# Optimization experiments

Hardware: AMD Instinct MI355X
Metric: run time of the kernel (lower is better)

Reference implementation:

```python
import math
import jax, jax.numpy as jnp
import numpy as np

L, H, C, T = 6, 16, 1024, 256   # layers, heads, n_embd, context steps (seq = 3T)
NACT, D_FF, B = 80, 4096, 4

def _conv(x, w, b, s, p):
    y = jax.lax.conv_general_dilated(x, w, (s, s), [(p, p), (p, p)],
                                     dimension_numbers=('NCHW', 'OIHW', 'NCHW'))
    return y + b[None, :, None, None]

def _ln(x, g, b):
    m = x.mean(-1, keepdims=True)
    v = ((x - m) ** 2).mean(-1, keepdims=True)
    return (x - m) / jnp.sqrt(v + 1e-5) * g + b

def _forward(states, rtgs, meta_states, circuit_feas,
             conv1_w, conv1_b, conv2_w, conv2_b, conv3_w, conv3_b,
             enc_w, enc_b, meta_w1, meta_b1, meta_w2, meta_b2,
             ret_w, ret_b, act_emb, pos_emb, gpos_emb,
             ln1_g, ln1_b, ln2_g, ln2_b,
             Wq, bq, Wk, bk, Wv, bv, Wo, bo,
             Wm1, bm1, Wm2, bm2, lnf_g, lnf_b, head_w,
             actions, timesteps):
    Bb, Tl = states.shape[0], states.shape[1]
    # state CNN encoder: (B*T, 8, 8, 10) -> 16 feats -> Linear(16, C-4)
    s = states.reshape(-1, 8, 8, 10)
    h = jax.nn.relu(_conv(s, conv1_w, conv1_b, 2, 1))
    h = jax.nn.relu(_conv(h, conv2_w, conv2_b, 2, 1))
    h = jax.nn.relu(_conv(h, conv3_w, conv3_b, 2, 1))
    se = h.reshape(h.shape[0], -1) @ enc_w + enc_b                    # (B*T, C-4)
    me = jax.nn.relu(meta_states.reshape(-1, 4) @ meta_w1 + meta_b1) @ meta_w2 + meta_b2
    state_emb = jnp.tanh(jnp.concatenate([se, me], axis=1)).reshape(Bb, Tl, C)
    # circuit embedding is computed then zeroed in source (no_circuit_emb=True) -> no effect
    rtg_emb = jnp.tanh(rtgs @ ret_w + ret_b)                          # (B, T, C)
    act_e = act_emb[actions[..., 0]]                                  # (B, T, C)
    # interleave (rtg, state, action) per timestep -> (B, 3T, C)
    tok = jnp.stack([rtg_emb, state_emb, act_e], axis=2).reshape(Bb, 3 * Tl, C)
    pos = gpos_emb[0, timesteps[:, 0, 0]][:, None, :] + pos_emb[:, :3 * Tl, :]
    x = tok + pos
    mask = jnp.tril(jnp.ones((3 * Tl, 3 * Tl), bool))
    d = C // H
    for i in range(L):
        hx = _ln(x, ln1_g[i], ln1_b[i])
        q = (hx @ Wq[i] + bq[i]).reshape(Bb, 3 * Tl, H, d)
        k = (hx @ Wk[i] + bk[i]).reshape(Bb, 3 * Tl, H, d)
        v = (hx @ Wv[i] + bv[i]).reshape(Bb, 3 * Tl, H, d)
        att = jnp.einsum('bqhd,bkhd->bhqk', q, k) / math.sqrt(d)
        att = jax.nn.softmax(jnp.where(mask, att, -jnp.inf), axis=-1)
        y = jnp.einsum('bhqk,bkhd->bqhd', att, v).reshape(Bb, 3 * Tl, C)
        x = x + (y @ Wo[i] + bo[i])
        h2 = _ln(x, ln2_g[i], ln2_b[i])
        x = x + (jax.nn.gelu(h2 @ Wm1[i] + bm1[i], approximate=False) @ Wm2[i] + bm2[i])
    logits = _ln(x, lnf_g, lnf_b) @ head_w                            # (B, 3T, NACT)
    return logits[:, 1::3, :]                                         # predictions at state tokens

def setup_inputs():
    ks = iter(jax.random.split(jax.random.key(0), 64))
    def W(*shape):
        return jax.random.normal(next(ks), shape, jnp.float32) * 0.02
    return {
        'states': jax.random.normal(next(ks), (B, T, 640), jnp.float32),
        'rtgs': jax.random.normal(next(ks), (B, T, 1), jnp.float32),
        'meta_states': jax.random.normal(next(ks), (B, T, 4), jnp.float32),
        'circuit_feas': jax.random.normal(next(ks), (B, 768), jnp.float32),
        'conv1_w': W(16, 8, 8, 8), 'conv1_b': jnp.zeros(16),
        'conv2_w': W(32, 16, 4, 4), 'conv2_b': jnp.zeros(32),
        'conv3_w': W(16, 32, 3, 3), 'conv3_b': jnp.zeros(16),
        'enc_w': W(16, C - 4), 'enc_b': jnp.zeros(C - 4),
        'meta_w1': W(4, 32), 'meta_b1': jnp.zeros(32),
        'meta_w2': W(32, 4), 'meta_b2': jnp.zeros(4),
        'ret_w': W(1, C), 'ret_b': jnp.zeros(C),
        'act_emb': W(NACT, C),
        'pos_emb': W(1, 3 * T + 1, C), 'gpos_emb': W(1, T + 1, C),
        'ln1_g': jnp.ones((L, C)), 'ln1_b': jnp.zeros((L, C)),
        'ln2_g': jnp.ones((L, C)), 'ln2_b': jnp.zeros((L, C)),
        'Wq': W(L, C, C), 'bq': jnp.zeros((L, C)),
        'Wk': W(L, C, C), 'bk': jnp.zeros((L, C)),
        'Wv': W(L, C, C), 'bv': jnp.zeros((L, C)),
        'Wo': W(L, C, C), 'bo': jnp.zeros((L, C)),
        'Wm1': W(L, C, D_FF), 'bm1': jnp.zeros((L, D_FF)),
        'Wm2': W(L, D_FF, C), 'bm2': jnp.zeros((L, C)),
        'lnf_g': jnp.ones(C), 'lnf_b': jnp.zeros(C),
        'head_w': W(C, NACT),
        'actions': jax.random.randint(next(ks), (B, T, 1), 0, NACT),
        'timesteps': jax.random.randint(next(ks), (B, 1, 1), 0, T + 1),
    }

def reference(states, rtgs, meta_states, circuit_feas,
              conv1_w, conv1_b, conv2_w, conv2_b, conv3_w, conv3_b,
              enc_w, enc_b, meta_w1, meta_b1, meta_w2, meta_b2,
              ret_w, ret_b, act_emb, pos_emb, gpos_emb,
              ln1_g, ln1_b, ln2_g, ln2_b,
              Wq, bq, Wk, bk, Wv, bv, Wo, bo,
              Wm1, bm1, Wm2, bm2, lnf_g, lnf_b, head_w,
              actions, timesteps):
    return _forward(states, rtgs, meta_states, circuit_feas,
                    conv1_w, conv1_b, conv2_w, conv2_b, conv3_w, conv3_b,
                    enc_w, enc_b, meta_w1, meta_b1, meta_w2, meta_b2,
                    ret_w, ret_b, act_emb, pos_emb, gpos_emb,
                    ln1_g, ln1_b, ln2_g, ln2_b,
                    Wq, bq, Wk, bk, Wv, bv, Wo, bo,
                    Wm1, bm1, Wm2, bm2, lnf_g, lnf_b, head_w,
                    actions, timesteps)
```

## Files before the change

### kernel.cpp

```cpp
#include <hip/hip_runtime.h>
#include <hip/hip_bf16.h>


#define S_LEN 768
#define C_DIM 1024
#define NHEAD 16
#define HDIM 64
#define BATCH 4
#define TCTX 256
#define DFF 4096
#define NACT 80
#define MROWS (BATCH * S_LEN)

typedef __attribute__((ext_vector_type(4))) float f32x4;
typedef __attribute__((ext_vector_type(8))) short bf16x8;
typedef __attribute__((ext_vector_type(8))) _Float16 f16x8;

static __device__ __forceinline__ unsigned short f2bf(float f) {
    unsigned int u = __float_as_uint(f);
    u += 0x7FFF + ((u >> 16) & 1);
    return (unsigned short)(u >> 16);
}
static __device__ __forceinline__ float bf2f(unsigned short h) {
    return __uint_as_float(((unsigned int)h) << 16);
}
static __device__ __forceinline__ unsigned short f2h(float f) {
    _Float16 h = (_Float16)f;
    return __builtin_bit_cast(unsigned short, h);
}

static __device__ __forceinline__ void gload16(void* l, const void* g) {
    __builtin_amdgcn_global_load_lds(
        (__attribute__((address_space(1))) void*)(g),
        (__attribute__((address_space(3))) void*)(l), 16, 0, 0);
}

__global__ __launch_bounds__(256) void transpose_w_kernel(
    const float* __restrict__ Wq, const float* __restrict__ Wk,
    const float* __restrict__ Wv, const float* __restrict__ Wo,
    const float* __restrict__ Wm1, const float* __restrict__ Wm2,
    unsigned short* __restrict__ Wb)
{
    const int t = blockIdx.x;
    const float* src; unsigned short* dst; int K, N, kt, nt;
    if (t < 1024) {
        const int m = t >> 8, tile = t & 255;
        src = (m == 0) ? Wq : (m == 1) ? Wk : (m == 2) ? Wv : Wo;
        dst = Wb + (size_t)m * 1048576;
        K = 1024; N = 1024; kt = tile >> 4; nt = tile & 15;
    } else if (t < 2048) {
        const int tile = t - 1024;
        src = Wm1; dst = Wb + (size_t)4 * 1048576;
        K = 1024; N = 4096; kt = tile >> 6; nt = tile & 63;
    } else {
        const int tile = t - 2048;
        src = Wm2; dst = Wb + (size_t)8 * 1048576;
        K = 4096; N = 1024; kt = tile >> 4; nt = tile & 15;
    }
    const int k0 = kt * 64, n0 = nt * 64;
    __shared__ float Ls[64][65];

    const int r = threadIdx.x >> 2, p = threadIdx.x & 3;
    #pragma unroll
    for (int i = 0; i < 4; ++i)
        *(float4*)&Ls[r][p * 16 + i * 4] =
            *(const float4*)&src[(size_t)(k0 + r) * N + n0 + p * 16 + i * 4];
    __syncthreads();

    unsigned short __align__(16) h[16];
    #pragma unroll
    for (int i = 0; i < 16; ++i) h[i] = f2bf(Ls[p * 16 + i][r]);
    unsigned short* d = dst + (size_t)(n0 + r) * K + k0 + p * 16;
    *(uint4*)d       = *(uint4*)&h[0];
    *(uint4*)(d + 8) = *(uint4*)&h[8];
}

__global__ __launch_bounds__(256) void embed_kernel(
    const float* __restrict__ states, const float* __restrict__ rtgs,
    const float* __restrict__ meta,
    const float* __restrict__ c1w, const float* __restrict__ c1b,
    const float* __restrict__ c2w, const float* __restrict__ c2b,
    const float* __restrict__ c3w, const float* __restrict__ c3b,
    const float* __restrict__ encw, const float* __restrict__ encb,
    const float* __restrict__ mw1, const float* __restrict__ mb1,
    const float* __restrict__ mw2, const float* __restrict__ mb2,
    const float* __restrict__ retw, const float* __restrict__ retb,
    const float* __restrict__ aemb, const float* __restrict__ pos,
    const float* __restrict__ gpos,
    const int* __restrict__ actions, const int* __restrict__ timesteps,
    float* __restrict__ X)
{
    const int n = blockIdx.x;
    const int b = n >> 8, t = n & 255;
    const int tid = threadIdx.x;

    __shared__ float sin_[640];
    __shared__ float h1[96];
    __shared__ float h2[32];
    __shared__ float feat[16];
    __shared__ float hidm[32];
    __shared__ float mer[4];

    for (int e = tid; e < 640; e += 256)
        sin_[e] = states[(size_t)n * 640 + e];
    __syncthreads();

    if (tid < 96) {
        int o = tid / 6, rem = tid % 6, oh = rem / 3, ow = rem % 3;
        float a = c1b[o];
        for (int ci = 0; ci < 8; ++ci)
            for (int kh = 0; kh < 8; ++kh) {
                int ih = oh * 2 - 1 + kh;
                if (ih < 0 || ih >= 8) continue;
                for (int kw = 0; kw < 8; ++kw) {
                    int iw = ow * 2 - 1 + kw;
                    if (iw < 0 || iw >= 10) continue;
                    a += c1w[((o * 8 + ci) * 8 + kh) * 8 + kw] * sin_[ci * 80 + ih * 10 + iw];
                }
            }
        h1[tid] = fmaxf(a, 0.f);
    }
    if (tid < 32) {
        float a = mb1[tid];
        for (int i = 0; i < 4; ++i)
            a += meta[(size_t)n * 4 + i] * mw1[i * 32 + tid];
        hidm[tid] = fmaxf(a, 0.f);
    }
    __syncthreads();

    if (tid < 32) {
        float a = c2b[tid];
        for (int ci = 0; ci < 16; ++ci)
            for (int kh = 0; kh < 4; ++kh) {
                int ih = -1 + kh;
                if (ih < 0 || ih >= 2) continue;
                for (int kw = 0; kw < 4; ++kw) {
                    int iw = -1 + kw;
                    if (iw < 0 || iw >= 3) continue;
                    a += c2w[((tid * 16 + ci) * 4 + kh) * 4 + kw] * h1[ci * 6 + ih * 3 + iw];
                }
            }
        h2[tid] = fmaxf(a, 0.f);
    }
    __syncthreads();

    if (tid < 16) {
        float a = c3b[tid];
        for (int ci = 0; ci < 32; ++ci)
            a += c3w[(tid * 32 + ci) * 9 + 4] * h2[ci];
        feat[tid] = fmaxf(a, 0.f);
    }
    if (tid < 4) {
        float a = mb2[tid];
        for (int j = 0; j < 32; ++j) a += hidm[j] * mw2[j * 4 + tid];
        mer[tid] = a;
    }
    __syncthreads();

    const float r = rtgs[n];
    const int a_idx = actions[n];
    const int g = timesteps[b];
    const size_t xbase = ((size_t)b * S_LEN + 3 * t) * C_DIM;

    for (int c = tid; c < C_DIM; c += 256) {
        float se;
        if (c < 1020) {
            float acc = encb[c];
            #pragma unroll
            for (int k = 0; k < 16; ++k) acc += feat[k] * encw[k * 1020 + c];
            se = acc;
        } else {
            se = mer[c - 1020];
        }
        const float st = tanhf(se);
        const float rt = tanhf(r * retw[c] + retb[c]);
        const float ae = aemb[(size_t)a_idx * C_DIM + c];
        const float gp = gpos[(size_t)g * C_DIM + c];
        X[xbase + c]             = rt + gp + pos[(size_t)(3 * t + 0) * C_DIM + c];
        X[xbase + C_DIM + c]     = st + gp + pos[(size_t)(3 * t + 1) * C_DIM + c];
        X[xbase + 2 * C_DIM + c] = ae + gp + pos[(size_t)(3 * t + 2) * C_DIM + c];
    }
}

__global__ __launch_bounds__(256) void ln_bf16_kernel(
    const float* __restrict__ in, unsigned short* __restrict__ out,
    const float* __restrict__ gw, const float* __restrict__ bw)
{
    const int row = blockIdx.x * 4 + (threadIdx.x >> 6);
    const int lane = threadIdx.x & 63;
    const float* x = in + (size_t)row * C_DIM;

    float4 v[4];
    float s = 0.f;
    #pragma unroll
    for (int j = 0; j < 4; ++j) {
        v[j] = *(const float4*)&x[lane * 4 + j * 256];
        s += (v[j].x + v[j].y) + (v[j].z + v[j].w);
    }
    #pragma unroll
    for (int o = 1; o < 64; o <<= 1) s += __shfl_xor(s, o, 64);
    const float mean = s * (1.0f / 1024.0f);

    float s2 = 0.f;
    #pragma unroll
    for (int j = 0; j < 4; ++j) {
        float dx = v[j].x - mean, dy = v[j].y - mean;
        float dz = v[j].z - mean, dw = v[j].w - mean;
        s2 += (dx * dx + dy * dy) + (dz * dz + dw * dw);
    }
    #pragma unroll
    for (int o = 1; o < 64; o <<= 1) s2 += __shfl_xor(s2, o, 64);
    const float inv = rsqrtf(s2 * (1.0f / 1024.0f) + 1e-5f);

    #pragma unroll
    for (int j = 0; j < 4; ++j) {
        const int c = lane * 4 + j * 256;
        ushort4 o4;
        o4.x = f2bf((v[j].x - mean) * inv * gw[c + 0] + bw[c + 0]);
        o4.y = f2bf((v[j].y - mean) * inv * gw[c + 1] + bw[c + 1]);
        o4.z = f2bf((v[j].z - mean) * inv * gw[c + 2] + bw[c + 2]);
        o4.w = f2bf((v[j].w - mean) * inv * gw[c + 3] + bw[c + 3]);
        *(ushort4*)&out[(size_t)row * C_DIM + c] = o4;
    }
}

__device__ __forceinline__ void gemm_core(
    const unsigned short* __restrict__ A, const unsigned short* __restrict__ Bt,
    int row0, int col0, int ldk, int nk, f32x4 (&acc)[4][4])
{
    __shared__ __align__(16) unsigned short As0[4][128][8];
    __shared__ __align__(16) unsigned short As1[4][128][8];
    __shared__ __align__(16) unsigned short As2[4][128][8];
    __shared__ __align__(16) unsigned short Bs0[4][128][8];
    __shared__ __align__(16) unsigned short Bs1[4][128][8];
    __shared__ __align__(16) unsigned short Bs2[4][128][8];

    const int tid = threadIdx.x;
    const int ar  = tid & 63, akg = tid >> 6;
    const int lane = tid & 63, w = tid >> 6;
    const int rwl = (w >> 1) * 64, cwl = (w & 1) * 64;
    const int mi = lane & 15, kg = lane >> 4;

    const unsigned short* pa = A + (size_t)(row0 + ar) * ldk + akg * 8;
    const unsigned short* pb = Bt + (size_t)(col0 + ar) * ldk + akg * 8;
    const size_t rstep = (size_t)64 * ldk;

    gload16(&As0[akg][ar][0],      pa);
    gload16(&As0[akg][ar + 64][0], pa + rstep);
    gload16(&Bs0[akg][ar][0],      pb);
    gload16(&Bs0[akg][ar + 64][0], pb + rstep);
    gload16(&As1[akg][ar][0],      pa + 32);
    gload16(&As1[akg][ar + 64][0], pa + rstep + 32);
    gload16(&Bs1[akg][ar][0],      pb + 32);
    gload16(&Bs1[akg][ar + 64][0], pb + rstep + 32);

#define GEMM_STEP(AC, BC, AP, BP, KK, VM, PF)                              \
    {                                                                      \
        asm volatile("s_waitcnt vmcnt(" #VM ")" ::: "memory");             \
        __builtin_amdgcn_s_barrier();                                      \
        __builtin_amdgcn_sched_barrier(0);                                 \
        if (PF) {                                                          \
            const unsigned short* ga = pa + (size_t)((KK) + 2) * 32;       \
            const unsigned short* gb = pb + (size_t)((KK) + 2) * 32;       \
            gload16(&AP[akg][ar][0],      ga);                             \
            gload16(&AP[akg][ar + 64][0], ga + rstep);                     \
            gload16(&BP[akg][ar][0],      gb);                             \
            gload16(&BP[akg][ar + 64][0], gb + rstep);                     \
        }                                                                  \
        bf16x8 af[4], bfr[4];                                              \
        _Pragma("unroll")                                                  \
        for (int i = 0; i < 4; ++i) {                                      \
            af[i]  = *(const bf16x8*)&AC[kg][rwl + i * 16 + mi][0];        \
            bfr[i] = *(const bf16x8*)&BC[kg][cwl + i * 16 + mi][0];        \
        }                                                                  \
        __builtin_amdgcn_s_setprio(1);                                     \
        _Pragma("unroll")                                                  \
        for (int ri = 0; ri < 4; ++ri)                                     \
            _Pragma("unroll")                                              \
            for (int ci = 0; ci < 4; ++ci)                                 \
                acc[ri][ci] = __builtin_amdgcn_mfma_f32_16x16x32_bf16(     \
                    af[ri], bfr[ci], acc[ri][ci], 0, 0, 0);                \
        __builtin_amdgcn_s_setprio(0);                                     \
    }

    int k = 0;
    while (k + 4 < nk) {
        GEMM_STEP(As0, Bs0, As2, Bs2, k,     4, 1)
        GEMM_STEP(As1, Bs1, As0, Bs0, k + 1, 4, 1)
        GEMM_STEP(As2, Bs2, As1, Bs1, k + 2, 4, 1)
        k += 3;
    }
    GEMM_STEP(As0, Bs0, As2, Bs2, k,     4, 0)
    GEMM_STEP(As1, Bs1, As0, Bs0, k + 1, 0, 0)
#undef GEMM_STEP
}

__global__ __launch_bounds__(256) void mfma_gemm_up(
    const unsigned short* __restrict__ A, const unsigned short* __restrict__ Bt,
    const float* __restrict__ bias, unsigned short* __restrict__ outb,
    int N, int K)
{
    const int h = blockIdx.x + (blockIdx.y << 5);
    const int xcd = h & 7, s = h >> 3;
    const int col0 = (s & 31) * 128;
    const int row0 = (xcd + 8 * (s >> 5)) * 128;

    f32x4 acc[4][4] = {};
    gemm_core(A, Bt, row0, col0, K, K >> 5, acc);

    const int lane = threadIdx.x & 63, w = threadIdx.x >> 6;
    const int rwl = (w >> 1) * 64, cwl = (w & 1) * 64;
    const int mi = lane & 15, kg = lane >> 4;

    #pragma unroll
    for (int ri = 0; ri < 4; ++ri)
        #pragma unroll
        for (int ci = 0; ci < 4; ++ci)
            #pragma unroll
            for (int j = 0; j < 4; ++j) {
                const int row = row0 + rwl + ri * 16 + kg * 4 + j;
                const int col = col0 + cwl + ci * 16 + mi;
                float v = acc[ri][ci][j] + bias[col];
                v = 0.5f * v * (1.0f + erff(v * 0.70710678118f));
                outb[(size_t)row * N + col] = f2bf(v);
            }
}

__global__ __launch_bounds__(256) void mfma_gemm_ressplit(
    const unsigned short* __restrict__ A, const unsigned short* __restrict__ Bt,
    const float* __restrict__ bias, float* __restrict__ X,
    int N, int K)
{
    const int h = blockIdx.x + (blockIdx.y << 3) + blockIdx.z * 192;
    const int xcd = h & 7, s = h >> 3;
    const int ks = s & 3;
    const int col0 = ((s >> 2) & 7) * 128;
    const int row0 = (xcd + 8 * (s >> 5)) * 128;

    const int kseg = K >> 2;
    f32x4 acc[4][4] = {};
    gemm_core(A + (size_t)ks * kseg, Bt + (size_t)ks * kseg,
              row0, col0, K, kseg >> 5, acc);

    const int lane = threadIdx.x & 63, w = threadIdx.x >> 6;
    const int rwl = (w >> 1) * 64, cwl = (w & 1) * 64;
    const int mi = lane & 15, kg = lane >> 4;

    #pragma unroll
    for (int ri = 0; ri < 4; ++ri)
        #pragma unroll
        for (int ci = 0; ci < 4; ++ci)
            #pragma unroll
            for (int j = 0; j < 4; ++j) {
                const int row = row0 + rwl + ri * 16 + kg * 4 + j;
                const int col = col0 + cwl + ci * 16 + mi;
                float v = acc[ri][ci][j] + (ks == 0 ? bias[col] : 0.f);
                atomicAdd(&X[(size_t)row * N + col], v);
            }
}

__global__ __launch_bounds__(256) void mfma_gemm_qkvt(
    const unsigned short* __restrict__ Xb, const unsigned short* __restrict__ Wb,
    const float* __restrict__ bq, const float* __restrict__ bk,
    const float* __restrict__ bv,
    unsigned short* __restrict__ Qh, unsigned short* __restrict__ Kh,
    unsigned short* __restrict__ Vt)
{
    const int h = blockIdx.x;
    const unsigned short *A, *Bt;
    int row0, col0, grp = -1;

    if (h < 384) {
        const int xcd = h & 7, s = h >> 3;
        const int x = s & 15;
        const int y = xcd + 8 * (s >> 4);
        grp = x >> 3;
        A = Xb; Bt = Wb + (size_t)grp * 1048576;
        row0 = y * 128; col0 = (x & 7) * 128;
    } else {
        const int j = h - 384;
        const int xcd = j & 7, s = j >> 3;
        A = Wb + (size_t)2 * 1048576; Bt = Xb;
        row0 = xcd * 128;
        col0 = s * 128;
    }

    f32x4 acc[4][4] = {};
    gemm_core(A, Bt, row0, col0, C_DIM, 32, acc);

    const int lane = threadIdx.x & 63, w = threadIdx.x >> 6;
    const int rwl = (w >> 1) * 64, cwl = (w & 1) * 64;
    const int mi = lane & 15, kg = lane >> 4;

    if (grp >= 0) {
        const float* bias = grp == 0 ? bq : bk;
        unsigned short* out = grp == 0 ? Qh : Kh;
        const float scale = grp == 0 ? 0.125f : 1.0f;
        #pragma unroll
        for (int ri = 0; ri < 4; ++ri)
            #pragma unroll
            for (int ci = 0; ci < 4; ++ci)
                #pragma unroll
                for (int j = 0; j < 4; ++j) {
                    const int row = row0 + rwl + ri * 16 + kg * 4 + j;
                    const int col = col0 + cwl + ci * 16 + mi;
                    out[(size_t)row * C_DIM + col] =
                        f2h((acc[ri][ci][j] + bias[col]) * scale);
                }
    } else {
        #pragma unroll
        for (int ri = 0; ri < 4; ++ri)
            #pragma unroll
            for (int ci = 0; ci < 4; ++ci)
                #pragma unroll
                for (int j = 0; j < 4; ++j) {
                    const int row = row0 + rwl + ri * 16 + kg * 4 + j;
                    const int col = col0 + cwl + ci * 16 + mi;
                    Vt[(size_t)row * MROWS + col] = f2h(acc[ri][ci][j] + bv[row]);
                }
    }
}

__global__ __launch_bounds__(256) void attn_mfma(
    const unsigned short* __restrict__ Qh, const unsigned short* __restrict__ Kh,
    const unsigned short* __restrict__ Vt, unsigned short* __restrict__ Yb)
{
    const int hw = blockIdx.x + 12 * (blockIdx.y + 16 * blockIdx.z);
    const int xcd = hw & 7, s = hw >> 3;
    const int qt = 11 - (s % 12);
    const int pair = xcd + 8 * (s / 12);
    const int h = pair & 15, b = pair >> 4;

    const int tid = threadIdx.x;
    const int lane = tid & 63, w = tid >> 6;
    const int mi = lane & 15, kg = lane >> 4;
    const int q0 = qt * 64;

    __shared__ __align__(16) char ldsraw[24576];
    unsigned short* Ks = (unsigned short*)ldsraw;
    unsigned short* Vs = (unsigned short*)(ldsraw + 8192);
    unsigned short* Ps = (unsigned short*)(ldsraw + 16384);
    float* Ob = (float*)ldsraw;

    const size_t qkbase = (size_t)b * S_LEN * C_DIM + (size_t)h * HDIM;
    const unsigned short* Kbase = Kh + qkbase;
    const unsigned short* Vbase = Vt + (size_t)h * HDIM * MROWS + (size_t)b * S_LEN;

    f16x8 QA0, QA1;
    {
        const unsigned short* qp = Qh + qkbase + (size_t)(q0 + w * 16 + mi) * C_DIM + kg * 8;
        QA0 = *(const f16x8*)qp;
        QA1 = *(const f16x8*)(qp + 32);
    }

    const int srow = tid >> 3, sc16 = tid & 7;
    const int dch = (sc16 ^ (srow & 7)) << 3;

    float mrow[4], lrow[4], alj[4];
    f32x4 Oacc[4];
    #pragma unroll
    for (int j = 0; j < 4; ++j) { mrow[j] = -1e30f; lrow[j] = 0.f; }
    #pragma unroll
    for (int df = 0; df < 4; ++df) Oacc[df] = (f32x4){0.f, 0.f, 0.f, 0.f};

    uint4 rk0, rk1, rv0, rv1;
    {
        const unsigned short* kp = Kbase + (size_t)srow * C_DIM + sc16 * 8;
        rk0 = *(const uint4*)kp;
        rk1 = *(const uint4*)(kp + (size_t)32 * C_DIM);
        const unsigned short* vp = Vbase + (size_t)srow * MROWS + sc16 * 8;
        rv0 = *(const uint4*)vp;
        rv1 = *(const uint4*)(vp + (size_t)32 * MROWS);
    }

    for (int kt = 0; kt <= qt; ++kt) {
        __syncthreads();
        *(uint4*)&Ks[srow * 64 + dch]        = rk0;
        *(uint4*)&Ks[(srow + 32) * 64 + dch] = rk1;
        *(uint4*)&Vs[srow * 64 + dch]        = rv0;
        *(uint4*)&Vs[(srow + 32) * 64 + dch] = rv1;
        if (kt < qt) {
            const unsigned short* kp = Kbase + (size_t)((kt + 1) * 64 + srow) * C_DIM + sc16 * 8;
            rk0 = *(const uint4*)kp;
            rk1 = *(const uint4*)(kp + (size_t)32 * C_DIM);
            const unsigned short* vp = Vbase + (size_t)srow * MROWS + (kt + 1) * 64 + sc16 * 8;
            rv0 = *(const uint4*)vp;
            rv1 = *(const uint4*)(vp + (size_t)32 * MROWS);
        }
        __syncthreads();

        f32x4 sa[4];
        #pragma unroll
        for (int kf = 0; kf < 4; ++kf) {
            const int key = kf * 16 + mi;
            const unsigned short* kr = Ks + key * 64;
            const f16x8 kb0 = *(const f16x8*)(kr + ((kg ^ (key & 7)) << 3));
            const f16x8 kb1 = *(const f16x8*)(kr + (((4 + kg) ^ (key & 7)) << 3));
            f32x4 z = {0.f, 0.f, 0.f, 0.f};
            z = __builtin_amdgcn_mfma_f32_16x16x32_f16(QA0, kb0, z, 0, 0, 0);
            sa[kf] = __builtin_amdgcn_mfma_f32_16x16x32_f16(QA1, kb1, z, 0, 0, 0);
        }

        if (kt == qt) {
            #pragma unroll
            for (int kf = 0; kf < 4; ++kf)
                #pragma unroll
                for (int j = 0; j < 4; ++j)
                    if (kf * 16 + mi > w * 16 + kg * 4 + j) sa[kf][j] = -1e30f;
        }

        #pragma unroll
        for (int j = 0; j < 4; ++j) {
            float rm = fmaxf(fmaxf(sa[0][j], sa[1][j]), fmaxf(sa[2][j], sa[3][j]));
            rm = fmaxf(rm, __shfl_xor(rm, 1, 16));
            rm = fmaxf(rm, __shfl_xor(rm, 2, 16));
            rm = fmaxf(rm, __shfl_xor(rm, 4, 16));
            rm = fmaxf(rm, __shfl_xor(rm, 8, 16));
            const float mn = fmaxf(mrow[j], rm);
            alj[j] = __expf(mrow[j] - mn);
            mrow[j] = mn;
            const float p0 = __expf(sa[0][j] - mn);
            const float p1 = __expf(sa[1][j] - mn);
            const float p2 = __expf(sa[2][j] - mn);
            const float p3 = __expf(sa[3][j] - mn);
            const int prow = w * 16 + kg * 4 + j;
            unsigned short* pr = Ps + prow * 64;
            const int sw = prow & 7, hi = mi >> 3, lo = mi & 7;
            pr[(((0 + hi) ^ sw) << 3) + lo] = f2h(p0);
            pr[(((2 + hi) ^ sw) << 3) + lo] = f2h(p1);
            pr[(((4 + hi) ^ sw) << 3) + lo] = f2h(p2);
            pr[(((6 + hi) ^ sw) << 3) + lo] = f2h(p3);
            float rs = p0 + p1 + p2 + p3;
            rs += __shfl_xor(rs, 1, 16);
            rs += __shfl_xor(rs, 2, 16);
            rs += __shfl_xor(rs, 4, 16);
            rs += __shfl_xor(rs, 8, 16);
            lrow[j] = lrow[j] * alj[j] + rs;
        }

        const unsigned short* pp = Ps + (w * 16 + mi) * 64;
        const int psw = mi & 7;
        const f16x8 PA0 = *(const f16x8*)(pp + ((kg ^ psw) << 3));
        const f16x8 PA1 = *(const f16x8*)(pp + (((4 + kg) ^ psw) << 3));
        #pragma unroll
        for (int df = 0; df < 4; ++df) {
            const int d = df * 16 + mi;
            const unsigned short* vr = Vs + d * 64;
            const f16x8 vb0 = *(const f16x8*)(vr + ((kg ^ (d & 7)) << 3));
            const f16x8 vb1 = *(const f16x8*)(vr + (((4 + kg) ^ (d & 7)) << 3));
            f32x4 o = Oacc[df];
            o[0] *= alj[0]; o[1] *= alj[1]; o[2] *= alj[2]; o[3] *= alj[3];
            o = __builtin_amdgcn_mfma_f32_16x16x32_f16(PA0, vb0, o, 0, 0, 0);
            Oacc[df] = __builtin_amdgcn_mfma_f32_16x16x32_f16(PA1, vb1, o, 0, 0, 0);
        }
    }

    __syncthreads();
    float inv[4];
    #pragma unroll
    for (int j = 0; j < 4; ++j) inv[j] = 1.0f / lrow[j];
    #pragma unroll
    for (int df = 0; df < 4; ++df)
        #pragma unroll
        for (int j = 0; j < 4; ++j)
            Ob[(w * 16 + kg * 4 + j) * 68 + df * 16 + mi] = Oacc[df][j] * inv[j];
    __syncthreads();

    const int orow = tid >> 2, oc0 = (tid & 3) * 16;
    unsigned short __align__(16) hx[16];
    #pragma unroll
    for (int i = 0; i < 16; ++i) hx[i] = f2bf(Ob[orow * 68 + oc0 + i]);
    unsigned short* yp = Yb + qkbase + (size_t)(q0 + orow) * C_DIM + oc0;
    *(uint4*)yp       = *(uint4*)&hx[0];
    *(uint4*)(yp + 8) = *(uint4*)&hx[8];
}

__global__ __launch_bounds__(256) void head_kernel(
    const unsigned short* __restrict__ Xb, const float* __restrict__ hw,
    float* __restrict__ out)
{
    const int n = blockIdx.x;
    const int b = n >> 8, t = n & 255;
    const int tid = threadIdx.x;
    __shared__ float rowv[C_DIM];

    const unsigned short* x = Xb + ((size_t)b * S_LEN + 3 * t + 1) * C_DIM;
    #pragma unroll
    for (int j = 0; j < 4; ++j) rowv[tid + j * 256] = bf2f(x[tid + j * 256]);
    __syncthreads();

    if (tid < NACT) {
        float a = 0.f;
        for (int k = 0; k < C_DIM; ++k) a += rowv[k] * hw[k * NACT + tid];
        out[(size_t)n * NACT + tid] = a;
    }
}

extern "C" void kernel_launch(void* const* d_in, const int* in_sizes, int n_in,
                              void* d_out, int out_size, void* d_ws, size_t ws_size,
                              hipStream_t stream) {
    const float* states  = (const float*)d_in[0];
    const float* rtgs    = (const float*)d_in[1];
    const float* meta    = (const float*)d_in[2];
    const float* c1w = (const float*)d_in[4];
    const float* c1b = (const float*)d_in[5];
    const float* c2w = (const float*)d_in[6];
    const float* c2b = (const float*)d_in[7];
    const float* c3w = (const float*)d_in[8];
    const float* c3b = (const float*)d_in[9];
    const float* encw = (const float*)d_in[10];
    const float* encb = (const float*)d_in[11];
    const float* mw1 = (const float*)d_in[12];
    const float* mb1 = (const float*)d_in[13];
    const float* mw2 = (const float*)d_in[14];
    const float* mb2 = (const float*)d_in[15];
    const float* retw = (const float*)d_in[16];
    const float* retb = (const float*)d_in[17];
    const float* aemb = (const float*)d_in[18];
    const float* pos  = (const float*)d_in[19];
    const float* gpos = (const float*)d_in[20];
    const float* ln1g = (const float*)d_in[21];
    const float* ln1b = (const float*)d_in[22];
    const float* ln2g = (const float*)d_in[23];
    const float* ln2b = (const float*)d_in[24];
    const float* Wq = (const float*)d_in[25];
    const float* bq = (const float*)d_in[26];
    const float* Wk = (const float*)d_in[27];
    const float* bk = (const float*)d_in[28];
    const float* Wv = (const float*)d_in[29];
    const float* bv = (const float*)d_in[30];
    const float* Wo = (const float*)d_in[31];
    const float* bo = (const float*)d_in[32];
    const float* Wm1 = (const float*)d_in[33];
    const float* bm1 = (const float*)d_in[34];
    const float* Wm2 = (const float*)d_in[35];
    const float* bm2 = (const float*)d_in[36];
    const float* lnfg = (const float*)d_in[37];
    const float* lnfb = (const float*)d_in[38];
    const float* hw   = (const float*)d_in[39];
    const int* actions   = (const int*)d_in[40];
    const int* timesteps = (const int*)d_in[41];

    float* out = (float*)d_out;

    char* wsc = (char*)d_ws;
    const size_t SLABB = (size_t)MROWS * C_DIM * 4;
    float* X  = (float*)wsc;
    unsigned short* Qh = (unsigned short*)(wsc + SLABB);
    unsigned short* Kh = Qh + (size_t)MROWS * C_DIM;
    unsigned short* Vt = (unsigned short*)(wsc + 2 * SLABB);
    unsigned short* Hb = (unsigned short*)(wsc + SLABB);
    unsigned short* Xb = (unsigned short*)(wsc + 4 * SLABB);
    unsigned short* Yb = (unsigned short*)(wsc + 4 * SLABB + SLABB / 2);
    unsigned short* Wb = (unsigned short*)(wsc + 5 * SLABB);

    embed_kernel<<<BATCH * TCTX, 256, 0, stream>>>(
        states, rtgs, meta, c1w, c1b, c2w, c2b, c3w, c3b, encw, encb,
        mw1, mb1, mw2, mb2, retw, retb, aemb, pos, gpos, actions, timesteps, X);

    const dim3 gres(8, 24, 4);
    const dim3 g4096(32, 24);
    const dim3 gattn(12, NHEAD, BATCH);

    for (int i = 0; i < 6; ++i) {
        const size_t wOff = (size_t)i * C_DIM * C_DIM;
        const size_t bOff = (size_t)i * C_DIM;
        const size_t m1Off = (size_t)i * C_DIM * DFF;

        transpose_w_kernel<<<3072, 256, 0, stream>>>(
            Wq + wOff, Wk + wOff, Wv + wOff, Wo + wOff, Wm1 + m1Off, Wm2 + m1Off, Wb);

        ln_bf16_kernel<<<MROWS / 4, 256, 0, stream>>>(X, Xb, ln1g + bOff, ln1b + bOff);
        mfma_gemm_qkvt<<<576, 256, 0, stream>>>(
            Xb, Wb, bq + bOff, bk + bOff, bv + bOff, Qh, Kh, Vt);
        attn_mfma<<<gattn, 256, 0, stream>>>(Qh, Kh, Vt, Yb);
        mfma_gemm_ressplit<<<gres, 256, 0, stream>>>(
            Yb, Wb + (size_t)3 * 1048576, bo + bOff, X, C_DIM, C_DIM);
        ln_bf16_kernel<<<MROWS / 4, 256, 0, stream>>>(X, Xb, ln2g + bOff, ln2b + bOff);
        mfma_gemm_up<<<g4096, 256, 0, stream>>>(
            Xb, Wb + (size_t)4 * 1048576, bm1 + (size_t)i * DFF, Hb, DFF, C_DIM);
        mfma_gemm_ressplit<<<gres, 256, 0, stream>>>(
            Hb, Wb + (size_t)8 * 1048576, bm2 + bOff, X, C_DIM, DFF);
    }

    ln_bf16_kernel<<<MROWS / 4, 256, 0, stream>>>(X, Xb, lnfg, lnfb);
    head_kernel<<<BATCH * TCTX, 256, 0, stream>>>(Xb, hw, out);
}
```

Before: 2.308 ms.

## Replace atomic split-K residual adds with two partial buffers reduced in LayerNorm

The output-projection and MLP-down GEMMs now split K two ways and write plain stores into two partial fp32 buffers, instead of splitting four ways and issuing atomicAdd into the residual. The following LayerNorm kernel sums X with both partials, writes X back and produces the bf16 normalized output, so the residual update is folded into a pass that already reads X. The GEMM pipeline loop is generalized to handle any number of k-steps with runtime wait conditions. This removes atomic traffic but halves the grid's K-parallelism, adds partial-buffer writes and reads, and requires a reworked workspace layout that overlaps the partial buffers with Qh, Vt and Wb.

```diff
diff --git a/kernel.cpp b/kernel.cpp
--- a/kernel.cpp
+++ b/kernel.cpp
@@ -224,6 +224,58 @@
     }
 }
 
+__global__ __launch_bounds__(256) void ln_red_bf16_kernel(
+    float* __restrict__ X,
+    const float* __restrict__ P0, const float* __restrict__ P1,
+    unsigned short* __restrict__ out,
+    const float* __restrict__ gw, const float* __restrict__ bw)
+{
+    const int row = blockIdx.x * 4 + (threadIdx.x >> 6);
+    const int lane = threadIdx.x & 63;
+    const size_t rb = (size_t)row * C_DIM;
+
+    float4 v[4];
+    float s = 0.f;
+    #pragma unroll
+    for (int j = 0; j < 4; ++j) {
+        const int c = lane * 4 + j * 256;
+        float4 a = *(const float4*)&X[rb + c];
+        float4 p = *(const float4*)&P0[rb + c];
+        float4 q = *(const float4*)&P1[rb + c];
+        v[j].x = a.x + p.x + q.x;
+        v[j].y = a.y + p.y + q.y;
+        v[j].z = a.z + p.z + q.z;
+        v[j].w = a.w + p.w + q.w;
+        *(float4*)&X[rb + c] = v[j];
+        s += (v[j].x + v[j].y) + (v[j].z + v[j].w);
+    }
+    #pragma unroll
+    for (int o = 1; o < 64; o <<= 1) s += __shfl_xor(s, o, 64);
+    const float mean = s * (1.0f / 1024.0f);
+
+    float s2 = 0.f;
+    #pragma unroll
+    for (int j = 0; j < 4; ++j) {
+        float dx = v[j].x - mean, dy = v[j].y - mean;
+        float dz = v[j].z - mean, dw = v[j].w - mean;
+        s2 += (dx * dx + dy * dy) + (dz * dz + dw * dw);
+    }
+    #pragma unroll
+    for (int o = 1; o < 64; o <<= 1) s2 += __shfl_xor(s2, o, 64);
+    const float inv = rsqrtf(s2 * (1.0f / 1024.0f) + 1e-5f);
+
+    #pragma unroll
+    for (int j = 0; j < 4; ++j) {
+        const int c = lane * 4 + j * 256;
+        ushort4 o4;
+        o4.x = f2bf((v[j].x - mean) * inv * gw[c + 0] + bw[c + 0]);
+        o4.y = f2bf((v[j].y - mean) * inv * gw[c + 1] + bw[c + 1]);
+        o4.z = f2bf((v[j].z - mean) * inv * gw[c + 2] + bw[c + 2]);
+        o4.w = f2bf((v[j].w - mean) * inv * gw[c + 3] + bw[c + 3]);
+        *(ushort4*)&out[rb + c] = o4;
+    }
+}
+
 __device__ __forceinline__ void gemm_core(
     const unsigned short* __restrict__ A, const unsigned short* __restrict__ Bt,
     int row0, int col0, int ldk, int nk, f32x4 (&acc)[4][4])
@@ -254,12 +306,13 @@
     gload16(&Bs1[akg][ar][0],      pb + 32);
     gload16(&Bs1[akg][ar + 64][0], pb + rstep + 32);
 
-#define GEMM_STEP(AC, BC, AP, BP, KK, VM, PF)                              \
+#define GEMM_STEP(AC, BC, AP, BP, KK)                                      \
     {                                                                      \
-        asm volatile("s_waitcnt vmcnt(" #VM ")" ::: "memory");             \
+        if ((KK) + 1 < nk) { asm volatile("s_waitcnt vmcnt(4)" ::: "memory"); } \
+        else               { asm volatile("s_waitcnt vmcnt(0)" ::: "memory"); } \
         __builtin_amdgcn_s_barrier();                                      \
         __builtin_amdgcn_sched_barrier(0);                                 \
-        if (PF) {                                                          \
+        if ((KK) + 2 < nk) {                                               \
             const unsigned short* ga = pa + (size_t)((KK) + 2) * 32;       \
             const unsigned short* gb = pb + (size_t)((KK) + 2) * 32;       \
             gload16(&AP[akg][ar][0],      ga);                             \
@@ -284,14 +337,12 @@
     }
 
     int k = 0;
-    while (k + 4 < nk) {
-        GEMM_STEP(As0, Bs0, As2, Bs2, k,     4, 1)
-        GEMM_STEP(As1, Bs1, As0, Bs0, k + 1, 4, 1)
-        GEMM_STEP(As2, Bs2, As1, Bs1, k + 2, 4, 1)
+    while (k < nk) {
+        GEMM_STEP(As0, Bs0, As2, Bs2, k)
+        if (k + 1 < nk) GEMM_STEP(As1, Bs1, As0, Bs0, k + 1)
+        if (k + 2 < nk) GEMM_STEP(As2, Bs2, As1, Bs1, k + 2)
         k += 3;
     }
-    GEMM_STEP(As0, Bs0, As2, Bs2, k,     4, 0)
-    GEMM_STEP(As1, Bs1, As0, Bs0, k + 1, 0, 0)
 #undef GEMM_STEP
 }
 
@@ -326,22 +377,24 @@
             }
 }
 
-__global__ __launch_bounds__(256) void mfma_gemm_ressplit(
+__global__ __launch_bounds__(256) void mfma_gemm_split2(
     const unsigned short* __restrict__ A, const unsigned short* __restrict__ Bt,
-    const float* __restrict__ bias, float* __restrict__ X,
+    const float* __restrict__ bias,
+    float* __restrict__ P0, float* __restrict__ P1,
     int N, int K)
 {
     const int h = blockIdx.x + (blockIdx.y << 3) + blockIdx.z * 192;
     const int xcd = h & 7, s = h >> 3;
-    const int ks = s & 3;
-    const int col0 = ((s >> 2) & 7) * 128;
-    const int row0 = (xcd + 8 * (s >> 5)) * 128;
-
-    const int kseg = K >> 2;
+    const int ks = s & 1;
+    const int col0 = ((s >> 1) & 7) * 128;
+    const int row0 = (xcd + 8 * (s >> 4)) * 128;
+
+    const int kseg = K >> 1;
     f32x4 acc[4][4] = {};
     gemm_core(A + (size_t)ks * kseg, Bt + (size_t)ks * kseg,
               row0, col0, K, kseg >> 5, acc);
 
+    float* P = ks == 0 ? P0 : P1;
     const int lane = threadIdx.x & 63, w = threadIdx.x >> 6;
     const int rwl = (w >> 1) * 64, cwl = (w & 1) * 64;
     const int mi = lane & 15, kg = lane >> 4;
@@ -354,8 +407,8 @@
             for (int j = 0; j < 4; ++j) {
                 const int row = row0 + rwl + ri * 16 + kg * 4 + j;
                 const int col = col0 + cwl + ci * 16 + mi;
-                float v = acc[ri][ci][j] + (ks == 0 ? bias[col] : 0.f);
-                atomicAdd(&X[(size_t)row * N + col], v);
+                P[(size_t)row * N + col] =
+                    acc[ri][ci][j] + (ks == 0 ? bias[col] : 0.f);
             }
 }
 
@@ -644,21 +697,25 @@
     float* out = (float*)d_out;
 
     char* wsc = (char*)d_ws;
-    const size_t SLABB = (size_t)MROWS * C_DIM * 4;
-    float* X  = (float*)wsc;
-    unsigned short* Qh = (unsigned short*)(wsc + SLABB);
-    unsigned short* Kh = Qh + (size_t)MROWS * C_DIM;
-    unsigned short* Vt = (unsigned short*)(wsc + 2 * SLABB);
-    unsigned short* Hb = (unsigned short*)(wsc + SLABB);
-    unsigned short* Xb = (unsigned short*)(wsc + 4 * SLABB);
-    unsigned short* Yb = (unsigned short*)(wsc + 4 * SLABB + SLABB / 2);
-    unsigned short* Wb = (unsigned short*)(wsc + 5 * SLABB);
+    const size_t MB = (size_t)1 << 20;
+    float*          X   = (float*)wsc;
+    unsigned short* Xb  = (unsigned short*)(wsc + 12 * MB);
+    unsigned short* Yb  = (unsigned short*)(wsc + 18 * MB);
+    unsigned short* Qh  = (unsigned short*)(wsc + 24 * MB);
+    unsigned short* Kh  = (unsigned short*)(wsc + 30 * MB);
+    unsigned short* Vt  = (unsigned short*)(wsc + 36 * MB);
+    float*          Po0 = (float*)(wsc + 24 * MB);
+    float*          Po1 = (float*)(wsc + 36 * MB);
+    unsigned short* Hb  = (unsigned short*)(wsc + 18 * MB);
+    float*          Pm0 = (float*)(wsc + 42 * MB);
+    float*          Pm1 = (float*)(wsc + 60 * MB);
+    unsigned short* Wb  = (unsigned short*)(wsc + 60 * MB);
 
     embed_kernel<<<BATCH * TCTX, 256, 0, stream>>>(
         states, rtgs, meta, c1w, c1b, c2w, c2b, c3w, c3b, encw, encb,
         mw1, mb1, mw2, mb2, retw, retb, aemb, pos, gpos, actions, timesteps, X);
 
-    const dim3 gres(8, 24, 4);
+    const dim3 gsplit(8, 24, 2);
     const dim3 g4096(32, 24);
     const dim3 gattn(12, NHEAD, BATCH);
 
@@ -667,22 +724,32 @@
         const size_t bOff = (size_t)i * C_DIM;
         const size_t m1Off = (size_t)i * C_DIM * DFF;
 
+        if (i == 0)
+            ln_bf16_kernel<<<MROWS / 4, 256, 0, stream>>>(
+                X, Xb, ln1g + bOff, ln1b + bOff);
+        else
+            ln_red_bf16_kernel<<<MROWS / 4, 256, 0, stream>>>(
+                X, Pm0, Pm1, Xb, ln1g + bOff, ln1b + bOff);
+
         transpose_w_kernel<<<3072, 256, 0, stream>>>(
             Wq + wOff, Wk + wOff, Wv + wOff, Wo + wOff, Wm1 + m1Off, Wm2 + m1Off, Wb);
 
-        ln_bf16_kernel<<<MROWS / 4, 256, 0, stream>>>(X, Xb, ln1g + bOff, ln1b + bOff);
         mfma_gemm_qkvt<<<576, 256, 0, stream>>>(
             Xb, Wb, bq + bOff, bk + bOff, bv + bOff, Qh, Kh, Vt);
         attn_mfma<<<gattn, 256, 0, stream>>>(Qh, Kh, Vt, Yb);
-        mfma_gemm_ressplit<<<gres, 256, 0, stream>>>(
-            Yb, Wb + (size_t)3 * 1048576, bo + bOff, X, C_DIM, C_DIM);
-        ln_bf16_kernel<<<MROWS / 4, 256, 0, stream>>>(X, Xb, ln2g + bOff, ln2b + bOff);
+
+        mfma_gemm_split2<<<gsplit, 256, 0, stream>>>(
+            Yb, Wb + (size_t)3 * 1048576, bo + bOff, Po0, Po1, C_DIM, C_DIM);
+        ln_red_bf16_kernel<<<MROWS / 4, 256, 0, stream>>>(
+            X, Po0, Po1, Xb, ln2g + bOff, ln2b + bOff);
+
         mfma_gemm_up<<<g4096, 256, 0, stream>>>(
             Xb, Wb + (size_t)4 * 1048576, bm1 + (size_t)i * DFF, Hb, DFF, C_DIM);
-        mfma_gemm_ressplit<<<gres, 256, 0, stream>>>(
-            Hb, Wb + (size_t)8 * 1048576, bm2 + bOff, X, C_DIM, DFF);
-    }
-
-    ln_bf16_kernel<<<MROWS / 4, 256, 0, stream>>>(X, Xb, lnfg, lnfb);
+        mfma_gemm_split2<<<gsplit, 256, 0, stream>>>(
+            Hb, Wb + (size_t)8 * 1048576, bm2 + bOff, Pm0, Pm1, C_DIM, DFF);
+    }
+
+    ln_red_bf16_kernel<<<MROWS / 4, 256, 0, stream>>>(
+        X, Pm0, Pm1, Xb, lnfg, lnfb);
     head_kernel<<<BATCH * TCTX, 256, 0, stream>>>(Xb, hw, out);
 }
```

Result: faster. 2.085 ms (-9.6%).
